# Optimization experiments

Measured on AMD Instinct MI355X. Metric: run time of the kernel, lower is better.

Reference implementation:

```python
import jax, jax.numpy as jnp
import numpy as np

S, TS, K, TK = 4, 2, 8, 8
EPS = 1e-5


def setup_inputs() -> dict:
    key = jax.random.key(0)
    ks = jax.random.split(key, 20)
    n, C, t, h, w = 8, 512, 8, 32, 32
    f = jnp.float32
    d = {}
    d["x"] = jax.random.normal(ks[0], (n, C, t, h, w), f)
    d["conv1_w"] = jax.random.normal(ks[1], (K, C), f) * 0.05
    d["conv1_b"] = jax.random.normal(ks[2], (K,), f) * 0.05
    d["bn1_g"] = jax.random.uniform(ks[3], (K,), f, 0.5, 1.5)
    d["bn1_b"] = jax.random.normal(ks[4], (K,), f) * 0.05
    d["bn1_m"] = jax.random.normal(ks[5], (K,), f) * 0.05
    d["bn1_v"] = jax.random.uniform(ks[6], (K,), f, 0.5, 1.5)
    d["convp_w"] = jax.random.normal(ks[7], (S * S * K, K, S), f) * 0.05
    d["convp_b"] = jax.random.normal(ks[8], (S * S * K,), f) * 0.05
    d["convq_w"] = jax.random.normal(ks[9], (S * S * K, K, S), f) * 0.05
    d["convq_b"] = jax.random.normal(ks[10], (S * S * K,), f) * 0.05
    d["convt_w"] = jax.random.normal(ks[11], (TS * TS * TK, K, TS), f) * 0.05
    d["convt_b"] = jax.random.normal(ks[12], (TS * TS * TK,), f) * 0.05
    d["conv2_w"] = jax.random.normal(ks[13], (C, C), f) * 0.05
    d["conv2_b"] = jax.random.normal(ks[14], (C,), f) * 0.05
    d["bn2_g"] = jax.random.uniform(ks[15], (C,), f, 0.5, 1.5)
    d["bn2_b"] = jax.random.normal(ks[16], (C,), f) * 0.05
    d["bn2_m"] = jax.random.normal(ks[17], (C,), f) * 0.05
    d["bn2_v"] = jax.random.uniform(ks[18], (C,), f, 0.5, 1.5)
    return d


def _bn(x, g, b, m, v):
    # inference-mode BatchNorm3d over channel axis 1
    sh = (1, -1, 1, 1, 1)
    return (x - m.reshape(sh)) * (g / jnp.sqrt(v + EPS)).reshape(sh) + b.reshape(sh)


def reference(x, conv1_w, conv1_b, bn1_g, bn1_b, bn1_m, bn1_v,
              convp_w, convp_b, convq_w, convq_b, convt_w, convt_b,
              conv2_w, conv2_b, bn2_g, bn2_b, bn2_m, bn2_v):
    n, C, t, h, w = x.shape
    s, ts, k, tk = S, TS, K, TK
    hb, wb, tb = h // s, w // s, t // ts
    # conv1 (1x1x1) + BN + ReLU -> (n,k,t,h,w)
    o = jnp.einsum('oc,ncthw->nothw', conv1_w, x) + conv1_b.reshape(1, -1, 1, 1, 1)
    o = jax.nn.relu(_bn(o, bn1_g, bn1_b, bn1_m, bn1_v))
    # adaptive max pools: (t,s,1) and (t,1,s) -> (n,k,t,s)
    rp = o.reshape(n, k, t, s, hb, w).max(axis=(4, 5))
    cp = o.reshape(n, k, t, h, s, wb).max(axis=(3, 5))
    # conv_p / conv_q: kernel [1,s,1] / [1,1,s] collapse the s axis
    p = (jnp.einsum('oci,ncti->not', convp_w, rp) + convp_b[None, :, None]).reshape(n, k, s, s, t)
    q = (jnp.einsum('oci,ncti->not', convq_w, cp) + convq_b[None, :, None]).reshape(n, k, s, s, t)
    p = jax.nn.softmax(p, axis=3)
    q = jax.nn.softmax(q, axis=2)
    # expand across C//k channel groups, move t forward -> (n,C,t,s,s)
    g = C // k
    P = jnp.broadcast_to(p.transpose(0, 1, 4, 2, 3)[:, :, None], (n, k, g, t, s, s)).reshape(n, C, t, s, s)
    Q = jnp.broadcast_to(q.transpose(0, 1, 4, 2, 3)[:, :, None], (n, k, g, t, s, s)).reshape(n, C, t, s, s)
    # y = kron(P, I_hb) @ x @ kron(Q, I_wb)  (resize_mat is kron with identity;
    # exploit block structure instead of materializing (n,C,t,h,h) matrices)
    xr = x.reshape(n, C, t, s, hb, w)
    y = jnp.einsum('nctab,nctbuw->nctauw', P, xr).reshape(n, C, t, h, w)
    yr = y.reshape(n, C, t, h, s, wb)
    y = jnp.einsum('ncthav,nctab->ncthbv', yr, Q).reshape(n, C, t, h, w)
    # temporal mixing: adaptive avg pool to (ts,1,1), conv_t, softmax, kron(TM, I_tb)
    tp = o.reshape(n, k, ts, tb, h, w).mean(axis=(3, 4, 5))  # (n,k,ts)
    tm = jnp.einsum('oci,nci->no', convt_w, tp) + convt_b[None, :]
    tm = jax.nn.softmax(tm.reshape(n, tk, ts, ts), axis=3)
    TM = jnp.broadcast_to(tm[:, :, None], (n, tk, C // tk, ts, ts)).reshape(n, C, ts, ts)
    y = jnp.einsum('ncab,ncbuhw->ncauhw', TM, y.reshape(n, C, ts, tb, h, w)).reshape(n, C, t, h, w)
    # conv2 (1x1x1) + BN + ReLU
    y = jnp.einsum('oc,ncthw->nothw', conv2_w, y) + conv2_b.reshape(1, -1, 1, 1, 1)
    return jax.nn.relu(_bn(y, bn2_g, bn2_b, bn2_m, bn2_v))
```

## Files before the change

kernel.cpp:

```cpp
#include <hip/hip_runtime.h>
#include <math.h>

#define EPS 1e-5f

typedef __bf16 bf16x8 __attribute__((ext_vector_type(8)));
typedef float f32x4 __attribute__((ext_vector_type(4)));

__device__ static inline unsigned short f2bf(float f) {
    unsigned u = __float_as_uint(f);
    unsigned r = (u + 0x7fffu + ((u >> 16) & 1u)) >> 16;
    return (unsigned short)r;
}

__device__ static inline void load_lds16(const void* g, void* l) {
    __builtin_amdgcn_global_load_lds(
        (const __attribute__((address_space(1))) unsigned int*)g,
        (__attribute__((address_space(3))) unsigned int*)l, 16, 0, 0);
}

__global__ __launch_bounds__(256) void k_w2cast(const float* __restrict__ w2,
                                                unsigned short* __restrict__ w2bf) {
    int i = (blockIdx.x * 256 + threadIdx.x) * 4;
    float4 v = *(const float4*)&w2[i];
    ushort4 o;
    o.x = f2bf(v.x); o.y = f2bf(v.y); o.z = f2bf(v.z); o.w = f2bf(v.w);
    *(ushort4*)&w2bf[i] = o;
}

__global__ __launch_bounds__(512) void k_conv1_pool(
    const float* __restrict__ x,  const float* __restrict__ w1,
    const float* __restrict__ b1, const float* __restrict__ g1,
    const float* __restrict__ bb1,const float* __restrict__ m1,
    const float* __restrict__ v1,
    float* __restrict__ rp, float* __restrict__ cp, float* __restrict__ tps)
{
    const int a   = blockIdx.x;
    const int t   = blockIdx.y;
    const int nn  = blockIdx.z;
    const int tid = threadIdx.x;
    const int wv  = tid >> 6;
    const int lane= tid & 63;

    __shared__ float part[8 * 8 * 256];

    const int cbase = __builtin_amdgcn_readfirstlane(wv) * 64;
    const float* xb = x + (size_t)nn * 512 * 8192 + (size_t)cbase * 8192
                        + t * 1024 + a * 256 + lane * 4;
    const float* wb = w1 + cbase;

    f32x4 acc[8];
#pragma unroll
    for (int k = 0; k < 8; k++) acc[k] = (f32x4){0.f, 0.f, 0.f, 0.f};

    for (int c = 0; c < 64; c += 8) {
        float4 xv[8];
#pragma unroll
        for (int cc = 0; cc < 8; cc++)
            xv[cc] = *(const float4*)(xb + (size_t)(c + cc) * 8192);
#pragma unroll
        for (int cc = 0; cc < 8; cc++) {
#pragma unroll
            for (int k = 0; k < 8; k++) {
                float wt = wb[k * 512 + c + cc];
                acc[k][0] += wt * xv[cc].x;
                acc[k][1] += wt * xv[cc].y;
                acc[k][2] += wt * xv[cc].z;
                acc[k][3] += wt * xv[cc].w;
            }
        }
    }
#pragma unroll
    for (int k = 0; k < 8; k++)
        *(f32x4*)&part[(wv * 8 + k) * 256 + lane * 4] = acc[k];
    __syncthreads();

    {
        const int k = tid >> 6;
        f32x4 s = (f32x4){0.f, 0.f, 0.f, 0.f};
#pragma unroll
        for (int g = 0; g < 8; g++) {
            f32x4 p = *(const f32x4*)&part[(g * 8 + k) * 256 + lane * 4];
            s[0] += p[0]; s[1] += p[1]; s[2] += p[2]; s[3] += p[3];
        }
        const float sc = g1[k] * rsqrtf(v1[k] + EPS);
        const float ba = (b1[k] - m1[k]) * sc + bb1[k];
        float o0 = fmaxf(s[0] * sc + ba, 0.f);
        float o1 = fmaxf(s[1] * sc + ba, 0.f);
        float o2 = fmaxf(s[2] * sc + ba, 0.f);
        float o3 = fmaxf(s[3] * sc + ba, 0.f);

        float m4 = fmaxf(fmaxf(o0, o1), fmaxf(o2, o3));
        float s4 = o0 + o1 + o2 + o3;

        float mr = m4;
#pragma unroll
        for (int m = 32; m >= 1; m >>= 1) mr = fmaxf(mr, __shfl_xor(mr, m, 64));
        if (lane == 0) rp[((nn * 8 + k) * 8 + t) * 4 + a] = mr;

        float mc = m4;
        mc = fmaxf(mc, __shfl_xor(mc, 1, 64));
        mc = fmaxf(mc, __shfl_xor(mc, 8, 64));
        mc = fmaxf(mc, __shfl_xor(mc, 16, 64));
        mc = fmaxf(mc, __shfl_xor(mc, 32, 64));
        if ((lane & 0x39) == 0)
            atomicMax((int*)&cp[((nn * 8 + k) * 8 + t) * 4 + (lane >> 1)],
                      __float_as_int(mc));

        float ss = s4;
#pragma unroll
        for (int m = 32; m >= 1; m >>= 1) ss += __shfl_xor(ss, m, 64);
        if (lane == 0) atomicAdd(&tps[(nn * 8 + k) * 2 + (t >> 2)], ss);
    }
}

__global__ __launch_bounds__(256) void k_pqtm(
    const float* __restrict__ rp, const float* __restrict__ cp,
    const float* __restrict__ tps,
    const float* __restrict__ pw, const float* __restrict__ pb,
    const float* __restrict__ qw, const float* __restrict__ qb,
    const float* __restrict__ tw, const float* __restrict__ tbv,
    float* __restrict__ P, float* __restrict__ Q, float* __restrict__ TM)
{
    const int nn  = blockIdx.x;
    const int tid = threadIdx.x;
    __shared__ float rps[256], cps[256], tpss[16];
    rps[tid] = rp[nn * 256 + tid];
    cps[tid] = cp[nn * 256 + tid];
    if (tid < 16) tpss[tid] = tps[nn * 16 + tid] * (1.0f / 4096.0f);
    __syncthreads();

    {
        int k = tid >> 5, a = (tid >> 3) & 3, t = tid & 7;
        float v[4];
#pragma unroll
        for (int b = 0; b < 4; b++) {
            int o = k * 16 + a * 4 + b;
            float s = pb[o];
#pragma unroll
            for (int c = 0; c < 8; c++)
#pragma unroll
                for (int i = 0; i < 4; i++)
                    s += pw[o * 32 + c * 4 + i] * rps[c * 32 + t * 4 + i];
            v[b] = s;
        }
        float mx = fmaxf(fmaxf(v[0], v[1]), fmaxf(v[2], v[3]));
        float e[4]; float sum = 0.f;
#pragma unroll
        for (int b = 0; b < 4; b++) { e[b] = expf(v[b] - mx); sum += e[b]; }
        float inv = 1.f / sum;
        int base = ((nn * 8 + k) * 8 + t) * 16 + a * 4;
#pragma unroll
        for (int b = 0; b < 4; b++) P[base + b] = e[b] * inv;
    }
    {
        int k = tid >> 5, b = (tid >> 3) & 3, t = tid & 7;
        float v[4];
#pragma unroll
        for (int a = 0; a < 4; a++) {
            int o = k * 16 + a * 4 + b;
            float s = qb[o];
#pragma unroll
            for (int c = 0; c < 8; c++)
#pragma unroll
                for (int i = 0; i < 4; i++)
                    s += qw[o * 32 + c * 4 + i] * cps[c * 32 + t * 4 + i];
            v[a] = s;
        }
        float mx = fmaxf(fmaxf(v[0], v[1]), fmaxf(v[2], v[3]));
        float e[4]; float sum = 0.f;
#pragma unroll
        for (int a = 0; a < 4; a++) { e[a] = expf(v[a] - mx); sum += e[a]; }
        float inv = 1.f / sum;
        int base = ((nn * 8 + k) * 8 + t) * 16 + b;
#pragma unroll
        for (int a = 0; a < 4; a++) Q[base + a * 4] = e[a] * inv;
    }
    if (tid < 16) {
        int kk = tid >> 1, a2 = tid & 1;
        float v[2];
#pragma unroll
        for (int b2 = 0; b2 < 2; b2++) {
            int o = kk * 4 + a2 * 2 + b2;
            float s = tbv[o];
#pragma unroll
            for (int c = 0; c < 8; c++)
#pragma unroll
                for (int i = 0; i < 2; i++)
                    s += tw[o * 16 + c * 2 + i] * tpss[c * 2 + i];
            v[b2] = s;
        }
        float mx = fmaxf(v[0], v[1]);
        float e0 = expf(v[0] - mx), e1 = expf(v[1] - mx);
        float inv = 1.f / (e0 + e1);
        TM[nn * 32 + kk * 4 + a2 * 2 + 0] = e0 * inv;
        TM[nn * 32 + kk * 4 + a2 * 2 + 1] = e1 * inv;
    }
}

__global__ __launch_bounds__(256) void k_mix(
    const float* __restrict__ x, const float* __restrict__ P,
    const float* __restrict__ Q, const float* __restrict__ TM,
    unsigned short* __restrict__ y3T)
{
    const int u2  = blockIdx.x >> 3;
    const int u   = blockIdx.x & 7;
    const int cg  = blockIdx.y;
    const int nn  = blockIdx.z;
    const int tid = threadIdx.x;

    __shared__ float xs[16384];
    __shared__ unsigned short ys[16384];

    const size_t xbase = (size_t)nn * 512 * 8192 + (size_t)cg * 64 * 8192;
#pragma unroll
    for (int rr = 0; rr < 16; rr++) {
        int id  = rr * 256 + tid;
        int row = id >> 3;
        int jw  = (id & 7) ^ (row & 7);
        int tt = row >> 8, b = (row >> 6) & 3, c = row & 63;
        const float* src = x + xbase + (size_t)c * 8192
                             + (u2 + 4 * tt) * 1024 + (b * 8 + u) * 32 + jw * 4;
        *(float4*)&xs[id * 4] = *(const float4*)src;
    }

    const int a = tid >> 6, c = tid & 63;
    float Pt[2][4], Qt[2][4][4];
#pragma unroll
    for (int tt = 0; tt < 2; tt++) {
        const float* Pb = &P[((nn * 8 + cg) * 8 + (u2 + 4 * tt)) * 16];
        const float* Qb = &Q[((nn * 8 + cg) * 8 + (u2 + 4 * tt)) * 16];
#pragma unroll
        for (int b = 0; b < 4; b++) Pt[tt][b] = Pb[a * 4 + b];
#pragma unroll
        for (int aw = 0; aw < 4; aw++)
#pragma unroll
            for (int bw = 0; bw < 4; bw++) Qt[tt][aw][bw] = Qb[aw * 4 + bw];
    }
    const float* TMb = &TM[nn * 32 + cg * 4];
    const float tm00 = TMb[0], tm01 = TMb[1], tm10 = TMb[2], tm11 = TMb[3];
    __syncthreads();

    float y1[2][32];
#pragma unroll
    for (int tt = 0; tt < 2; tt++) {
#pragma unroll
        for (int w = 0; w < 32; w++) y1[tt][w] = 0.f;
#pragma unroll
        for (int b = 0; b < 4; b++) {
            int row = (tt * 4 + b) * 64 + c;
            float pv = Pt[tt][b];
#pragma unroll
            for (int jw = 0; jw < 8; jw++) {
                int chunk = row * 8 + (jw ^ (c & 7));
                float4 xv = *(const float4*)&xs[chunk * 4];
                y1[tt][jw * 4 + 0] += pv * xv.x;
                y1[tt][jw * 4 + 1] += pv * xv.y;
                y1[tt][jw * 4 + 2] += pv * xv.z;
                y1[tt][jw * 4 + 3] += pv * xv.w;
            }
        }
    }
#pragma unroll
    for (int w = 0; w < 32; w++) {
        int bw = w >> 3, v = w & 7;
        float s0 = 0.f, s1 = 0.f;
#pragma unroll
        for (int aw = 0; aw < 4; aw++) {
            s0 += Qt[0][aw][bw] * y1[0][aw * 8 + v];
            s1 += Qt[1][aw][bw] * y1[1][aw * 8 + v];
        }
        ys[((0 + a) * 32 + w) * 64 + c] = f2bf(tm00 * s0 + tm01 * s1);
        ys[((4 + a) * 32 + w) * 64 + c] = f2bf(tm10 * s0 + tm11 * s1);
    }
    __syncthreads();

#pragma unroll
    for (int it = 0; it < 8; it++) {
        int id  = it * 256 + tid;
        int row = id >> 3, jc = id & 7;
        int tt = row >> 7, aa = (row >> 5) & 3, w = row & 31;
        int p = (u2 + 4 * tt) * 1024 + (aa * 8 + u) * 32 + w;
        uint4 val = *(const uint4*)&ys[id * 8];
        *(uint4*)&y3T[((size_t)nn * 8192 + p) * 512 + cg * 64 + jc * 8] = val;
    }
}

__global__ __launch_bounds__(256) void k_gemm2(
    const unsigned short* __restrict__ y3T,
    const unsigned short* __restrict__ w2bf,
    const float* __restrict__ b2, const float* __restrict__ g2,
    const float* __restrict__ bb2,const float* __restrict__ m2,
    const float* __restrict__ v2, float* __restrict__ out)
{
    const int ct  = blockIdx.x;
    const int pt  = blockIdx.y;
    const int nn  = blockIdx.z;
    const int tid = threadIdx.x;
    const int co0 = ct * 128, p0 = pt * 128;

    __shared__ unsigned short As[8192];
    __shared__ unsigned short Bs[8192];
    __shared__ float sc_s[128], ba_s[128];

    if (tid < 128) {
        int co = co0 + tid;
        float sc = g2[co] * rsqrtf(v2[co] + EPS);
        sc_s[tid] = sc;
        ba_s[tid] = (b2[co] - m2[co]) * sc + bb2[co];
    }

    const int lane = tid & 63, wv = tid >> 6;
    const int wr = wv >> 1, wc = wv & 1;
    const int ln15 = lane & 15, quad = lane >> 4;

    const int lrow = lane >> 3;
    const int jc   = (lane & 7) ^ lrow;

    f32x4 acc[4][4];
#pragma unroll
    for (int i = 0; i < 4; i++)
#pragma unroll
        for (int j = 0; j < 4; j++) acc[i][j] = (f32x4){0.f, 0.f, 0.f, 0.f};

    const unsigned short* Ag = w2bf + (size_t)co0 * 512;
    const unsigned short* Bg = y3T + ((size_t)nn * 8192 + p0) * 512;

    for (int c0 = 0; c0 < 512; c0 += 64) {
#pragma unroll
        for (int it = 0; it < 4; it++) {
            int rb = (wv * 4 + it) * 8;
            load_lds16(Ag + (size_t)(rb + lrow) * 512 + c0 + jc * 8,
                       &As[(wv * 4 + it) * 512]);
            load_lds16(Bg + (size_t)(rb + lrow) * 512 + c0 + jc * 8,
                       &Bs[(wv * 4 + it) * 512]);
        }
        __syncthreads();

#pragma unroll
        for (int ks = 0; ks < 2; ks++) {
            bf16x8 a[4], b[4];
#pragma unroll
            for (int mi = 0; mi < 4; mi++) {
                int row = wr * 64 + mi * 16 + ln15;
                int chunk = row * 8 + ((ks * 4 + quad) ^ (row & 7));
                a[mi] = *(const bf16x8*)&As[chunk * 8];
            }
#pragma unroll
            for (int pi = 0; pi < 4; pi++) {
                int row = wc * 64 + pi * 16 + ln15;
                int chunk = row * 8 + ((ks * 4 + quad) ^ (row & 7));
                b[pi] = *(const bf16x8*)&Bs[chunk * 8];
            }
#pragma unroll
            for (int mi = 0; mi < 4; mi++)
#pragma unroll
                for (int pi = 0; pi < 4; pi++)
                    acc[mi][pi] = __builtin_amdgcn_mfma_f32_16x16x32_bf16(
                        a[mi], b[pi], acc[mi][pi], 0, 0, 0);
        }
        __syncthreads();
    }

#pragma unroll
    for (int mi = 0; mi < 4; mi++) {
        int lco = wr * 64 + mi * 16 + quad * 4;
#pragma unroll
        for (int pi = 0; pi < 4; pi++) {
            int p = p0 + wc * 64 + pi * 16 + ln15;
#pragma unroll
            for (int r = 0; r < 4; r++) {
                float vv = acc[mi][pi][r] * sc_s[lco + r] + ba_s[lco + r];
                out[((size_t)nn * 512 + co0 + lco + r) * 8192 + p] =
                    fmaxf(vv, 0.f);
            }
        }
    }
}

extern "C" void kernel_launch(void* const* d_in, const int* in_sizes, int n_in,
                              void* d_out, int out_size, void* d_ws, size_t ws_size,
                              hipStream_t stream) {
    const float* x   = (const float*)d_in[0];
    const float* w1  = (const float*)d_in[1];
    const float* b1  = (const float*)d_in[2];
    const float* g1  = (const float*)d_in[3];
    const float* bb1 = (const float*)d_in[4];
    const float* m1  = (const float*)d_in[5];
    const float* v1  = (const float*)d_in[6];
    const float* pw  = (const float*)d_in[7];
    const float* pb  = (const float*)d_in[8];
    const float* qw  = (const float*)d_in[9];
    const float* qb  = (const float*)d_in[10];
    const float* tw  = (const float*)d_in[11];
    const float* tbv = (const float*)d_in[12];
    const float* w2  = (const float*)d_in[13];
    const float* b2  = (const float*)d_in[14];
    const float* g2  = (const float*)d_in[15];
    const float* bb2 = (const float*)d_in[16];
    const float* m2  = (const float*)d_in[17];
    const float* v2  = (const float*)d_in[18];

    float* ws  = (float*)d_ws;
    float* rp  = ws;
    float* cp  = ws + 2048;
    float* tps = ws + 4096;
    float* P   = ws + 8192;
    float* Q   = ws + 16384;
    float* TM  = ws + 24576;
    unsigned short* w2bf = (unsigned short*)(ws + 32768);
    unsigned short* y3T  = (unsigned short*)(ws + 163840);

    hipMemsetAsync(ws, 0, 4224 * sizeof(float), stream);

    k_w2cast<<<dim3(256), 256, 0, stream>>>(w2, w2bf);
    k_conv1_pool<<<dim3(4, 8, 8), 512, 0, stream>>>(x, w1, b1, g1, bb1, m1, v1,
                                                    rp, cp, tps);
    k_pqtm<<<dim3(8), 256, 0, stream>>>(rp, cp, tps, pw, pb, qw, qb, tw, tbv,
                                        P, Q, TM);
    k_mix<<<dim3(32, 8, 8), 256, 0, stream>>>(x, P, Q, TM, y3T);
    k_gemm2<<<dim3(4, 64, 8), 256, 0, stream>>>(y3T, w2bf, b2, g2, bb2, m2, v2,
                                                (float*)d_out);
}
```

Measured before the change: 365.6 us.

## Fuse w2 cast into conv1 kernel, halve mix channel tile, nontemporal output stores

The standalone bf16 cast kernel for conv2 weights is folded into the conv1/pool kernel, removing one launch. The mixing kernel now handles 32 channels per block instead of 64, doubling the grid and halving LDS use and per-thread registers (y1 shrinks from 64 to 32 floats), which should raise occupancy. The GEMM epilogue writes output with nontemporal stores to avoid polluting cache. Trade-offs: the mix kernel does more, smaller global writes per row, and the conv1 blocks take on extra work.

```diff
diff --git a/kernel.cpp b/kernel.cpp
--- a/kernel.cpp
+++ b/kernel.cpp
@@ -16,15 +16,6 @@
     __builtin_amdgcn_global_load_lds(
         (const __attribute__((address_space(1))) unsigned int*)g,
         (__attribute__((address_space(3))) unsigned int*)l, 16, 0, 0);
-}
-
-__global__ __launch_bounds__(256) void k_w2cast(const float* __restrict__ w2,
-                                                unsigned short* __restrict__ w2bf) {
-    int i = (blockIdx.x * 256 + threadIdx.x) * 4;
-    float4 v = *(const float4*)&w2[i];
-    ushort4 o;
-    o.x = f2bf(v.x); o.y = f2bf(v.y); o.z = f2bf(v.z); o.w = f2bf(v.w);
-    *(ushort4*)&w2bf[i] = o;
 }
 
 __global__ __launch_bounds__(512) void k_conv1_pool(
@@ -32,6 +23,7 @@
     const float* __restrict__ b1, const float* __restrict__ g1,
     const float* __restrict__ bb1,const float* __restrict__ m1,
     const float* __restrict__ v1,
+    const float* __restrict__ w2, unsigned short* __restrict__ w2bf,
     float* __restrict__ rp, float* __restrict__ cp, float* __restrict__ tps)
 {
     const int a   = blockIdx.x;
@@ -42,6 +34,16 @@
     const int lane= tid & 63;
 
     __shared__ float part[8 * 8 * 256];
+
+    {
+        int gid = (((nn * 8 + t) * 4 + a) * 512) + tid;
+        if (gid < 65536) {
+            float4 v = *(const float4*)&w2[gid * 4];
+            ushort4 o;
+            o.x = f2bf(v.x); o.y = f2bf(v.y); o.z = f2bf(v.z); o.w = f2bf(v.w);
+            *(ushort4*)&w2bf[gid * 4] = o;
+        }
+    }
 
     const int cbase = __builtin_amdgcn_readfirstlane(wv) * 64;
     const float* xb = x + (size_t)nn * 512 * 8192 + (size_t)cbase * 8192
@@ -207,28 +209,29 @@
     const int cg  = blockIdx.y;
     const int nn  = blockIdx.z;
     const int tid = threadIdx.x;
-
-    __shared__ float xs[16384];
-    __shared__ unsigned short ys[16384];
-
-    const size_t xbase = (size_t)nn * 512 * 8192 + (size_t)cg * 64 * 8192;
-#pragma unroll
-    for (int rr = 0; rr < 16; rr++) {
+    const int kc  = cg >> 1;
+
+    __shared__ float xs[8192];
+    __shared__ unsigned short ys[8192];
+
+    const size_t xbase = (size_t)nn * 512 * 8192 + (size_t)cg * 32 * 8192;
+#pragma unroll
+    for (int rr = 0; rr < 8; rr++) {
         int id  = rr * 256 + tid;
         int row = id >> 3;
         int jw  = (id & 7) ^ (row & 7);
-        int tt = row >> 8, b = (row >> 6) & 3, c = row & 63;
+        int tt = row >> 7, b = (row >> 5) & 3, c = row & 31;
         const float* src = x + xbase + (size_t)c * 8192
                              + (u2 + 4 * tt) * 1024 + (b * 8 + u) * 32 + jw * 4;
         *(float4*)&xs[id * 4] = *(const float4*)src;
     }
 
-    const int a = tid >> 6, c = tid & 63;
+    const int a = tid >> 6, vh = (tid >> 5) & 1, c = tid & 31;
     float Pt[2][4], Qt[2][4][4];
 #pragma unroll
     for (int tt = 0; tt < 2; tt++) {
-        const float* Pb = &P[((nn * 8 + cg) * 8 + (u2 + 4 * tt)) * 16];
-        const float* Qb = &Q[((nn * 8 + cg) * 8 + (u2 + 4 * tt)) * 16];
+        const float* Pb = &P[((nn * 8 + kc) * 8 + (u2 + 4 * tt)) * 16];
+        const float* Qb = &Q[((nn * 8 + kc) * 8 + (u2 + 4 * tt)) * 16];
 #pragma unroll
         for (int b = 0; b < 4; b++) Pt[tt][b] = Pb[a * 4 + b];
 #pragma unroll
@@ -236,52 +239,59 @@
 #pragma unroll
             for (int bw = 0; bw < 4; bw++) Qt[tt][aw][bw] = Qb[aw * 4 + bw];
     }
-    const float* TMb = &TM[nn * 32 + cg * 4];
+    const float* TMb = &TM[nn * 32 + kc * 4];
     const float tm00 = TMb[0], tm01 = TMb[1], tm10 = TMb[2], tm11 = TMb[3];
     __syncthreads();
 
-    float y1[2][32];
+    float y1[2][4][4];
+#pragma unroll
+    for (int tt = 0; tt < 2; tt++)
+#pragma unroll
+        for (int aw = 0; aw < 4; aw++)
+#pragma unroll
+            for (int vi = 0; vi < 4; vi++) y1[tt][aw][vi] = 0.f;
 #pragma unroll
     for (int tt = 0; tt < 2; tt++) {
 #pragma unroll
-        for (int w = 0; w < 32; w++) y1[tt][w] = 0.f;
-#pragma unroll
         for (int b = 0; b < 4; b++) {
-            int row = (tt * 4 + b) * 64 + c;
             float pv = Pt[tt][b];
-#pragma unroll
-            for (int jw = 0; jw < 8; jw++) {
-                int chunk = row * 8 + (jw ^ (c & 7));
-                float4 xv = *(const float4*)&xs[chunk * 4];
-                y1[tt][jw * 4 + 0] += pv * xv.x;
-                y1[tt][jw * 4 + 1] += pv * xv.y;
-                y1[tt][jw * 4 + 2] += pv * xv.z;
-                y1[tt][jw * 4 + 3] += pv * xv.w;
-            }
-        }
-    }
-#pragma unroll
-    for (int w = 0; w < 32; w++) {
-        int bw = w >> 3, v = w & 7;
-        float s0 = 0.f, s1 = 0.f;
-#pragma unroll
-        for (int aw = 0; aw < 4; aw++) {
-            s0 += Qt[0][aw][bw] * y1[0][aw * 8 + v];
-            s1 += Qt[1][aw][bw] * y1[1][aw * 8 + v];
-        }
-        ys[((0 + a) * 32 + w) * 64 + c] = f2bf(tm00 * s0 + tm01 * s1);
-        ys[((4 + a) * 32 + w) * 64 + c] = f2bf(tm10 * s0 + tm11 * s1);
+            int row = (tt * 4 + b) * 32 + c;
+#pragma unroll
+            for (int aw = 0; aw < 4; aw++) {
+                int slot = (aw * 2 + vh) ^ (c & 7);
+                float4 xv = *(const float4*)&xs[(row * 8 + slot) * 4];
+                y1[tt][aw][0] += pv * xv.x;
+                y1[tt][aw][1] += pv * xv.y;
+                y1[tt][aw][2] += pv * xv.z;
+                y1[tt][aw][3] += pv * xv.w;
+            }
+        }
+    }
+#pragma unroll
+    for (int bw = 0; bw < 4; bw++) {
+#pragma unroll
+        for (int vi = 0; vi < 4; vi++) {
+            float s0 = 0.f, s1 = 0.f;
+#pragma unroll
+            for (int aw = 0; aw < 4; aw++) {
+                s0 += Qt[0][aw][bw] * y1[0][aw][vi];
+                s1 += Qt[1][aw][bw] * y1[1][aw][vi];
+            }
+            int wout = bw * 8 + vh * 4 + vi;
+            ys[((0 + a) * 32 + wout) * 32 + c] = f2bf(tm00 * s0 + tm01 * s1);
+            ys[((4 + a) * 32 + wout) * 32 + c] = f2bf(tm10 * s0 + tm11 * s1);
+        }
     }
     __syncthreads();
 
 #pragma unroll
-    for (int it = 0; it < 8; it++) {
+    for (int it = 0; it < 4; it++) {
         int id  = it * 256 + tid;
-        int row = id >> 3, jc = id & 7;
+        int row = id >> 2, jc = id & 3;
         int tt = row >> 7, aa = (row >> 5) & 3, w = row & 31;
         int p = (u2 + 4 * tt) * 1024 + (aa * 8 + u) * 32 + w;
-        uint4 val = *(const uint4*)&ys[id * 8];
-        *(uint4*)&y3T[((size_t)nn * 8192 + p) * 512 + cg * 64 + jc * 8] = val;
+        uint4 val = *(const uint4*)&ys[row * 32 + jc * 8];
+        *(uint4*)&y3T[((size_t)nn * 8192 + p) * 512 + cg * 32 + jc * 8] = val;
     }
 }
 
@@ -369,9 +379,10 @@
             int p = p0 + wc * 64 + pi * 16 + ln15;
 #pragma unroll
             for (int r = 0; r < 4; r++) {
-                float vv = acc[mi][pi][r] * sc_s[lco + r] + ba_s[lco + r];
-                out[((size_t)nn * 512 + co0 + lco + r) * 8192 + p] =
-                    fmaxf(vv, 0.f);
+                float vv = fmaxf(acc[mi][pi][r] * sc_s[lco + r] + ba_s[lco + r],
+                                 0.f);
+                __builtin_nontemporal_store(
+                    vv, &out[((size_t)nn * 512 + co0 + lco + r) * 8192 + p]);
             }
         }
     }
@@ -412,12 +423,11 @@
 
     hipMemsetAsync(ws, 0, 4224 * sizeof(float), stream);
 
-    k_w2cast<<<dim3(256), 256, 0, stream>>>(w2, w2bf);
     k_conv1_pool<<<dim3(4, 8, 8), 512, 0, stream>>>(x, w1, b1, g1, bb1, m1, v1,
-                                                    rp, cp, tps);
+                                                    w2, w2bf, rp, cp, tps);
     k_pqtm<<<dim3(8), 256, 0, stream>>>(rp, cp, tps, pw, pb, qw, qb, tw, tbv,
                                         P, Q, TM);
-    k_mix<<<dim3(32, 8, 8), 256, 0, stream>>>(x, P, Q, TM, y3T);
+    k_mix<<<dim3(32, 16, 8), 256, 0, stream>>>(x, P, Q, TM, y3T);
     k_gemm2<<<dim3(4, 64, 8), 256, 0, stream>>>(y3T, w2bf, b2, g2, bb2, m2, v2,
                                                 (float*)d_out);
 }
```

New measurement: 347.9 us. -4.8%, faster.
